# Optimization experiments

Measured on AMD Instinct MI355X. Metric: run time of the kernel, lower is better.

The kernel has to match this reference:

```python
import jax, jax.numpy as jnp
import numpy as np

D_MODEL = 256
D_STATE = 64
MAX_CONCEPTS = 64
CENTROID_LR = 0.1
CREATE_THRESHOLD = 0.75
REFINE_THRESHOLD = 1.0
NEG_INF = -1e9


def _l2norm(v):
    # F.normalize with eps=1e-12
    n = jnp.sqrt(jnp.sum(v * v, axis=-1, keepdims=True))
    return v / jnp.maximum(n, 1e-12)


def setup_inputs() -> dict:
    key = jax.random.key(0)
    ks = jax.random.split(key, 6)
    B, T = 4, 1024
    x = jax.random.normal(ks[0], (B, T, D_MODEL), dtype=jnp.float32)
    s = 1.0 / np.sqrt(D_MODEL)
    Wq = jax.random.normal(ks[1], (D_MODEL, D_STATE), dtype=jnp.float32) * s
    Wk = jax.random.normal(ks[2], (D_MODEL, D_STATE), dtype=jnp.float32) * s
    Wv = jax.random.normal(ks[3], (D_MODEL, D_MODEL), dtype=jnp.float32) * s
    Wo = jax.random.normal(ks[4], (D_MODEL, D_MODEL), dtype=jnp.float32) * s
    return {
        "x": x,
        "Wq": Wq, "bq": jnp.zeros((D_STATE,), jnp.float32),
        "Wk": Wk, "bk": jnp.zeros((D_STATE,), jnp.float32),
        "Wv": Wv, "bv": jnp.zeros((D_MODEL,), jnp.float32),
        "Wo": Wo, "bo": jnp.zeros((D_MODEL,), jnp.float32),
        "logit_scale": jnp.float32(np.log(1.0 / np.sqrt(D_STATE))),
    }


def _forward(x, Wq, bq, Wk, bk, Wv, bv, Wo, bo, logit_scale):
    M = MAX_CONCEPTS
    # q is only ever used .detach()ed in the original; k is detached too.
    q_all = jax.lax.stop_gradient(_l2norm((x @ Wq + bq).astype(jnp.float32)))
    k_all = jax.lax.stop_gradient(_l2norm((x @ Wk + bk).astype(jnp.float32)))
    v_all = x @ Wv + bv
    scale = jnp.minimum(jnp.exp(logit_scale), 100.0)
    slot_ids = jnp.arange(M)

    def step(carry, inp):
        centroids, values, counts, n = carry  # [M,ds],[M,dm],[M], int32
        q_t, k_t, v_t = inp
        valid = slot_ids < n
        sims = centroids @ q_t                      # [M]
        scores = jnp.where(valid, sims, NEG_INF)
        weights = jax.nn.softmax(scores * scale)    # [M]
        has = n > 0
        z = jnp.where(has, weights @ values, jnp.zeros_like(v_t))
        sel = jnp.argmax(weights)
        sel_sim = sims[sel]
        v_sel = values[sel]
        residual = jnp.sqrt(jnp.mean(
            (jax.lax.stop_gradient(v_sel) - jax.lax.stop_gradient(v_t)) ** 2))
        refine = has & (n < M) & ((sel_sim < CREATE_THRESHOLD) | (residual > REFINE_THRESHOLD))
        do_add = ((~has) | refine) & (n < M)
        do_update = has & (~refine)
        # running-mean update of value memory; EMA + renormalize of centroid
        upd_c = jax.lax.stop_gradient(
            _l2norm((1.0 - CENTROID_LR) * centroids[sel] + CENTROID_LR * k_t))
        new_v = (v_sel * counts[sel] + v_t) / (counts[sel] + 1.0)
        centroids = centroids.at[sel].set(jnp.where(do_update, upd_c, centroids[sel]))
        values = values.at[sel].set(jnp.where(do_update, new_v, v_sel))
        counts = counts.at[sel].set(counts[sel] + do_update.astype(counts.dtype))
        # concept creation in slot n (sel < n always, so no collision)
        slot = jnp.minimum(n, M - 1)
        centroids = centroids.at[slot].set(jnp.where(do_add, k_t, centroids[slot]))
        values = values.at[slot].set(jnp.where(do_add, v_t, values[slot]))
        counts = counts.at[slot].set(jnp.where(do_add, 1.0, counts[slot]))
        n = n + do_add.astype(n.dtype)
        return (centroids, values, counts, n), z

    def run_seq(q, k, v):
        ds, dm = q.shape[-1], v.shape[-1]
        init = (jnp.zeros((M, ds), jnp.float32),
                jnp.zeros((M, dm), jnp.float32),
                jnp.zeros((M,), jnp.float32),
                jnp.int32(0))
        _, zs = jax.lax.scan(step, init, (q, k, v))
        return zs  # [T, dm]

    y = jax.vmap(run_seq)(q_all, k_all, v_all).astype(x.dtype)
    return y @ Wo + bo  # dropout p=0 -> identity


def reference(x, Wq, bq, Wk, bk, Wv, bv, Wo, bo, logit_scale):
    return _forward(x, Wq, bq, Wk, bk, Wv, bv, Wo, bo, logit_scale)
```

## Files before the change

kernel.cpp:

```cpp
#include <hip/hip_runtime.h>
#include <hip/hip_bf16.h>

#define D_MODEL 256
#define D_STATE 64
#define MCON    64
#define TLEN    1024
#define BATCH   4
#define NEG_INF -1e9f
#define PT      16
#define ZT      8

#define BAR() asm volatile("s_waitcnt lgkmcnt(0)\n\ts_barrier" ::: "memory")

template <int CTRL, int RM>
__device__ __forceinline__ float dpp_f(float x) {
    int xi = __float_as_int(x);
    int r  = __builtin_amdgcn_update_dpp(xi, xi, CTRL, RM, 0xf, false);
    return __int_as_float(r);
}
__device__ __forceinline__ float bcast_lane(float x, int lane) {
    return __int_as_float(__builtin_amdgcn_readlane(__float_as_int(x), lane));
}
__device__ __forceinline__ float wave_sum(float x) {
    x += dpp_f<0x111, 0xf>(x);
    x += dpp_f<0x112, 0xf>(x);
    x += dpp_f<0x114, 0xf>(x);
    x += dpp_f<0x118, 0xf>(x);
    x += dpp_f<0x142, 0xa>(x);
    x += dpp_f<0x143, 0xc>(x);
    return bcast_lane(x, 63);
}
__device__ __forceinline__ float wave_max(float x) {
    x = fmaxf(x, dpp_f<0x111, 0xf>(x));
    x = fmaxf(x, dpp_f<0x112, 0xf>(x));
    x = fmaxf(x, dpp_f<0x114, 0xf>(x));
    x = fmaxf(x, dpp_f<0x118, 0xf>(x));
    x = fmaxf(x, dpp_f<0x142, 0xa>(x));
    x = fmaxf(x, dpp_f<0x143, 0xc>(x));
    return bcast_lane(x, 63);
}
__device__ __forceinline__ int wave_argmax_fast(float lg, float mx) {
    const unsigned long long m = __ballot(lg == mx);
    return (int)(__ffsll((long long)m) - 1);
}
__device__ __forceinline__ float dpp_swap1(float x) {
    int xi = __float_as_int(x);
    return __int_as_float(__builtin_amdgcn_update_dpp(xi, xi, 0xB1, 0xf, 0xf, false));
}

__global__ __launch_bounds__(256) void proj_kernel(
    const float* __restrict__ x,
    const float* __restrict__ Wq, const float* __restrict__ bq,
    const float* __restrict__ Wk, const float* __restrict__ bk,
    const float* __restrict__ Wv, const float* __restrict__ bv,
    float* __restrict__ q_ws, float* __restrict__ k_ws, float* __restrict__ v_ws)
{
    const int tok0 = blockIdx.x * PT;
    const int tid  = threadIdx.x;
    __shared__ float sx[PT][D_MODEL];

    #pragma unroll
    for (int tt = 0; tt < PT; ++tt)
        sx[tt][tid] = x[(size_t)(tok0 + tt) * D_MODEL + tid];
    __syncthreads();

    {
        float acc[PT];
        #pragma unroll
        for (int tt = 0; tt < PT; ++tt) acc[tt] = 0.f;
        for (int i = 0; i < D_MODEL; ++i) {
            const float w = Wv[i * D_MODEL + tid];
            #pragma unroll
            for (int tt = 0; tt < PT; ++tt) acc[tt] += sx[tt][i] * w;
        }
        const float bvi = bv[tid];
        #pragma unroll
        for (int tt = 0; tt < PT; ++tt)
            v_ws[(size_t)(tok0 + tt) * D_MODEL + tid] = acc[tt] + bvi;
    }

    if (tid < 128) {
        const int j = tid & 63;
        const float* W  = (tid < 64) ? Wq : Wk;
        const float* bb = (tid < 64) ? bq : bk;
        float a[PT];
        #pragma unroll
        for (int tt = 0; tt < PT; ++tt) a[tt] = 0.f;
        for (int i = 0; i < D_MODEL; ++i) {
            const float w = W[i * D_STATE + j];
            #pragma unroll
            for (int tt = 0; tt < PT; ++tt) a[tt] += sx[tt][i] * w;
        }
        const float bbj = bb[j];
        #pragma unroll
        for (int tt = 0; tt < PT; ++tt) {
            const float av = a[tt] + bbj;
            float s2 = av * av;
            #pragma unroll
            for (int off = 1; off < 64; off <<= 1) s2 += __shfl_xor(s2, off, 64);
            const float nrm = fmaxf(sqrtf(s2), 1e-12f);
            const float o = av / nrm;
            if (tid < 64) q_ws[(size_t)(tok0 + tt) * D_STATE + j] = o;
            else          k_ws[(size_t)(tok0 + tt) * D_STATE + j] = o;
        }
    }
}

__global__ __launch_bounds__(256) void scan_kernel(
    const float* __restrict__ q_ws, const float* __restrict__ k_ws,
    const float* __restrict__ v_ws,
    float* __restrict__ sims_ws, int* __restrict__ n_ws,
    int* __restrict__ ver_ws, float* __restrict__ vlog_ws,
    const float* __restrict__ ls_p)
{
    const int b   = blockIdx.x;
    const int tid = threadIdx.x;
    const int l   = tid & 63;
    const int wv  = tid >> 6;
    const float scale = fminf(expf(ls_p[0]), 100.f);

    __shared__ __align__(16) float sV[MCON * D_MODEL];
    __shared__ __align__(16) float sQ[2][D_STATE];
    __shared__ __align__(16) float sK[2][D_STATE];
    __shared__ __align__(16) float sBuf[2][MCON];
    __shared__ __align__(16) float sS2[2][MCON];
    __shared__ float sFA[2];
    __shared__ int   sFlagChg[2];
    __shared__ int   sFlagUpd[2];

    const float4 zero4 = make_float4(0.f, 0.f, 0.f, 0.f);
    #pragma unroll
    for (int i = 0; i < 16; ++i) ((float4*)sV)[i * 256 + tid] = zero4;
    if (tid < MCON) { sBuf[0][tid] = 0.f; sS2[0][tid] = 0.f; }
    if (tid == 0) { sFA[0] = 0.f; sFlagChg[0] = -1; sFlagUpd[0] = 0; }

    const float* qg = q_ws + b * TLEN * D_STATE;
    const float* kg = k_ws + b * TLEN * D_STATE;
    const float* vg = v_ws + b * TLEN * D_MODEL;
    float* vlog_b   = vlog_ws + (size_t)b * (TLEN + 1) * D_MODEL;

    if (tid < 64) {
        *(float4*)&vlog_b[4 * l] = zero4;
        sQ[1][l] = qg[D_STATE + l];
        sK[0][l] = kg[l];
    }

    float qcur = 0.f, kcur = 0.f, qnx2 = 0.f, knx = 0.f;
    float fa_prev = 0.f;
    int   n0 = 0, ver0 = 0;
    if (wv == 0) {
        kcur = kg[l];
        qcur = qg[D_STATE + l];
        knx  = kg[D_STATE + l];
        qnx2 = qg[2 * D_STATE + l];
    }
    float  cnt_l = 0.f;
    int    n = 0, chg_prev = -1, upd_prev = 0;
    float4 vvt = zero4;
    if (wv == 1) vvt = *(const float4*)&vg[4 * l];
    const int brow = ((wv - 2) << 5) + (l >> 1);
    const int bh   = l & 1;
    float4 Creg[8];
    float4 tprev[8], kprev[8];
    float  s2prev = 0.f;
    #pragma unroll
    for (int c = 0; c < 8; ++c) { Creg[c] = zero4; tprev[c] = zero4; kprev[c] = zero4; }

    __syncthreads();

    for (int t = 0; t < TLEN; ++t) {
        const int token = b * TLEN + t;
        const int pc = t & 1, pn = 1 - pc;

        if (wv >= 2) {
            const int  chg  = sFlagChg[pc];
            const bool updf = sFlagUpd[pc] != 0;
            if (chg == brow) {
                const float rn = 1.f / fmaxf(sqrtf(s2prev), 1e-12f);
                #pragma unroll
                for (int c = 0; c < 8; ++c) {
                    Creg[c].x = updf ? tprev[c].x * rn : kprev[c].x;
                    Creg[c].y = updf ? tprev[c].y * rn : kprev[c].y;
                    Creg[c].z = updf ? tprev[c].z * rn : kprev[c].z;
                    Creg[c].w = updf ? tprev[c].w * rn : kprev[c].w;
                }
            }
            const float* qrow = &sQ[pn][32 * bh];
            const float* krow = &sK[pc][32 * bh];
            float pa = 0.f, pb = 0.f, sa = 0.f, sb = 0.f;
            #pragma unroll
            for (int c = 0; c < 8; ++c) {
                const float4 c4 = Creg[c];
                const float4 q4 = *(const float4*)(qrow + 4 * c);
                const float4 k4 = *(const float4*)(krow + 4 * c);
                float4 t4;
                t4.x = 0.9f * c4.x + 0.1f * k4.x;
                t4.y = 0.9f * c4.y + 0.1f * k4.y;
                t4.z = 0.9f * c4.z + 0.1f * k4.z;
                t4.w = 0.9f * c4.w + 0.1f * k4.w;
                if (c < 4) {
                    pa += c4.x * q4.x; pa += c4.y * q4.y;
                    pa += c4.z * q4.z; pa += c4.w * q4.w;
                    sa += t4.x * t4.x; sa += t4.y * t4.y;
                    sa += t4.z * t4.z; sa += t4.w * t4.w;
                } else {
                    pb += c4.x * q4.x; pb += c4.y * q4.y;
                    pb += c4.z * q4.z; pb += c4.w * q4.w;
                    sb += t4.x * t4.x; sb += t4.y * t4.y;
                    sb += t4.z * t4.z; sb += t4.w * t4.w;
                }
                tprev[c] = t4; kprev[c] = k4;
            }
            const float sd  = pa + pb;
            const float dot = sd + dpp_swap1(sd);
            const float ss  = sa + sb;
            const float s2  = ss + dpp_swap1(ss);
            s2prev = s2;
            if (bh == 0) { sBuf[pn][brow] = dot; sS2[pn][brow] = s2; }
        }

        if (wv == 0) {
            const int chg0 = sFlagChg[pc];
            const int upd0 = sFlagUpd[pc];
            n0  += (chg0 >= 0 && upd0 == 0) ? 1 : 0;
            if (l == chg0) ver0 = t;
            const float bufv0 = sBuf[pc][l];
            const int   ip0   = (chg0 < 0) ? 0 : chg0;
            const float s2v0  = sS2[pc][ip0];
            const float bdc0  = bcast_lane(bufv0, ip0);
            const float fupd0 = (0.9f * bdc0 + 0.1f * fa_prev)
                                / fmaxf(sqrtf(s2v0), 1e-12f);
            const float fsim0 = upd0 ? fupd0 : fa_prev;
            const float simv0 = (l == chg0) ? fsim0 : bufv0;
            sims_ws[(size_t)token * MCON + l] = simv0;
            ver_ws[(size_t)token * MCON + l]  = ver0;
            if (l == 0) n_ws[token] = n0;

            sQ[pc][l] = qnx2;
            sK[pn][l] = knx;
            const float fa = wave_sum(kcur * qcur);
            if (l == 0) sFA[pn] = fa;
            fa_prev = fa;
            kcur = knx; qcur = qnx2;
            const int tk2 = (t + 2 < TLEN) ? t + 2 : TLEN - 1;
            const int tq3 = (t + 3 < TLEN) ? t + 3 : TLEN - 1;
            knx  = kg[tk2 * D_STATE + l];
            qnx2 = qg[tq3 * D_STATE + l];
        }

        if (wv == 1) {
            const float4 vt = vvt;
            const int tk = (t + 1 < TLEN) ? t + 1 : t;
            vvt = *(const float4*)&vg[tk * D_MODEL + 4 * l];

            const int   ip   = (chg_prev < 0) ? 0 : chg_prev;
            const float bufv = sBuf[pc][l];
            const float s2v  = sS2[pc][ip];
            const float fa   = sFA[pc];
            const float bdc  = bcast_lane(bufv, ip);
            const float fupd = (0.9f * bdc + 0.1f * fa)
                               / fmaxf(sqrtf(s2v), 1e-12f);
            const float fsim = upd_prev ? fupd : fa;
            const float simv = (l == chg_prev) ? fsim : bufv;

            const float lg = ((l < n) ? simv : NEG_INF) * scale;
            const float mx = wave_max(lg);
            const int   sel    = wave_argmax_fast(lg, mx);
            const float selSim = bcast_lane(simv,  sel);
            const float cnt    = bcast_lane(cnt_l, sel);

            const float4 vs = *(const float4*)&sV[sel * D_MODEL + 4 * l];
            float r = (vs.x - vt.x) * (vs.x - vt.x)
                    + (vs.y - vt.y) * (vs.y - vt.y)
                    + (vs.z - vt.z) * (vs.z - vt.z)
                    + (vs.w - vt.w) * (vs.w - vt.w);
            const float residual = sqrtf(wave_sum(r) * (1.f / 256.f));

            const bool has = n > 0;
            const bool refine = has && (n < MCON) &&
                                (selSim < 0.75f || residual > 1.0f);
            const bool do_add    = ((!has) || refine) && (n < MCON);
            const bool do_update = has && !refine;
            const int  chg = do_update ? sel : n;

            float4 nv;
            nv.x = (vs.x * cnt + vt.x) / (cnt + 1.f);
            nv.y = (vs.y * cnt + vt.y) / (cnt + 1.f);
            nv.z = (vs.z * cnt + vt.z) / (cnt + 1.f);
            nv.w = (vs.w * cnt + vt.w) / (cnt + 1.f);
            float4 valV;
            valV.x = do_update ? nv.x : vt.x;
            valV.y = do_update ? nv.y : vt.y;
            valV.z = do_update ? nv.z : vt.z;
            valV.w = do_update ? nv.w : vt.w;
            *(float4*)&sV[chg * D_MODEL + 4 * l] = valV;
            *(float4*)&vlog_b[(size_t)(t + 1) * D_MODEL + 4 * l] = valV;

            if (l == 0) { sFlagChg[pn] = chg; sFlagUpd[pn] = do_update ? 1 : 0; }

            if (l == sel && do_update) cnt_l = cnt + 1.f;
            if (l == n   && do_add)    cnt_l = 1.f;
            n += do_add ? 1 : 0;
            chg_prev = chg; upd_prev = do_update ? 1 : 0;
        }

        BAR();
    }
}

__global__ __launch_bounds__(256) void zout_kernel(
    const float* __restrict__ sims_ws, const int* __restrict__ n_ws,
    const int* __restrict__ ver_ws, const float* __restrict__ vlog_ws,
    const float* __restrict__ Wo, const float* __restrict__ bo,
    float* __restrict__ out, const float* __restrict__ ls_p)
{
    const int tok0 = blockIdx.x * ZT;
    const int b    = tok0 >> 10;
    const int tid  = threadIdx.x;
    const int l    = tid & 63;
    const int wv   = tid >> 6;
    const float scale = fminf(expf(ls_p[0]), 100.f);

    __shared__ float sWt[ZT][MCON];
    __shared__ int   sVer[ZT][MCON];
    __shared__ int   sN[ZT];
    __shared__ float sy[ZT][D_MODEL];

    for (int tt = wv; tt < ZT; tt += 4) {
        const int token = tok0 + tt;
        const int nt = n_ws[token];
        if (l == 0) sN[tt] = nt;
        sVer[tt][l] = ver_ws[(size_t)token * MCON + l];
        const float simv = sims_ws[(size_t)token * MCON + l];
        const float lg = ((l < nt) ? simv : NEG_INF) * scale;
        const float mx = wave_max(lg);
        const float e  = expf(lg - mx);
        const float sm = wave_sum(e);
        sWt[tt][l] = e / sm;
    }
    __syncthreads();

    const float* base = vlog_ws + (size_t)b * (TLEN + 1) * D_MODEL;
    #pragma unroll
    for (int tt = 0; tt < ZT; ++tt) {
        float z = 0.f;
        const int ntc = sN[tt];
        if (ntc > 0) {
            #pragma unroll 8
            for (int m = 0; m < ntc; ++m) {
                const float wm = sWt[tt][m];
                z += wm * base[(size_t)sVer[tt][m] * D_MODEL + tid];
            }
        }
        sy[tt][tid] = z;
    }
    __syncthreads();

    float acc[ZT];
    #pragma unroll
    for (int tt = 0; tt < ZT; ++tt) acc[tt] = 0.f;
    for (int i = 0; i < D_MODEL; ++i) {
        const float wo = Wo[i * D_MODEL + tid];
        #pragma unroll
        for (int tt = 0; tt < ZT; ++tt) acc[tt] += sy[tt][i] * wo;
    }
    const float boi = bo[tid];
    #pragma unroll
    for (int tt = 0; tt < ZT; ++tt)
        out[(size_t)(tok0 + tt) * D_MODEL + tid] = acc[tt] + boi;
}

extern "C" void kernel_launch(void* const* d_in, const int* in_sizes, int n_in,
                              void* d_out, int out_size, void* d_ws, size_t ws_size,
                              hipStream_t stream)
{
    const float* x  = (const float*)d_in[0];
    const float* Wq = (const float*)d_in[1];
    const float* bq = (const float*)d_in[2];
    const float* Wk = (const float*)d_in[3];
    const float* bk = (const float*)d_in[4];
    const float* Wv = (const float*)d_in[5];
    const float* bv = (const float*)d_in[6];
    const float* Wo = (const float*)d_in[7];
    const float* bo = (const float*)d_in[8];
    const float* ls = (const float*)d_in[9];
    float* out = (float*)d_out;

    const int NTOK = BATCH * TLEN;
    char* ws = (char*)d_ws;
    size_t off = 0;
    float* q_ws    = (float*)(ws + off); off += (size_t)NTOK * D_STATE * 4;
    float* k_ws    = (float*)(ws + off); off += (size_t)NTOK * D_STATE * 4;
    float* v_ws    = (float*)(ws + off); off += (size_t)NTOK * D_MODEL * 4;
    float* sims_ws = (float*)(ws + off); off += (size_t)NTOK * MCON * 4;
    int*   ver_ws  = (int*)  (ws + off); off += (size_t)NTOK * MCON * 4;
    int*   n_ws    = (int*)  (ws + off); off += (size_t)NTOK * 4;
    float* vlog_ws = (float*)(ws + off);

    proj_kernel<<<NTOK / PT, 256, 0, stream>>>(x, Wq, bq, Wk, bk, Wv, bv,
                                               q_ws, k_ws, v_ws);
    scan_kernel<<<BATCH, 256, 0, stream>>>(q_ws, k_ws, v_ws,
                                           sims_ws, n_ws, ver_ws, vlog_ws, ls);
    zout_kernel<<<NTOK / ZT, 256, 0, stream>>>(sims_ws, n_ws, ver_ws, vlog_ws,
                                               Wo, bo, out, ls);
}
```

Baseline: 846.1 us.

## Fuse scan and output kernels with flag-based overlap of zout chunks

Merges the sequential scan kernel and the output projection kernel into one persistent launch. The first blocks run the per-batch scan and post release flags every 64 tokens, while the remaining blocks spin on those flags and compute softmax-weighted outputs and the Wo projection for finished chunks. The aim is to hide the output stage behind the long serial scan. This relies on all blocks being co-resident and adds spin-wait and fence overhead, with a fallback to separate launches when the workspace is too small.

After: 869.8 us. +2.8%, slower.

```diff
diff --git a/kernel.cpp b/kernel.cpp
--- a/kernel.cpp
+++ b/kernel.cpp
@@ -9,6 +9,9 @@
 #define NEG_INF -1e9f
 #define PT      16
 #define ZT      8
+#define ZUNITS  512
+#define NZB     508
+#define SMEM_BYTES 67616
 
 #define BAR() asm volatile("s_waitcnt lgkmcnt(0)\n\ts_barrier" ::: "memory")
 
@@ -46,6 +49,10 @@
 __device__ __forceinline__ float dpp_swap1(float x) {
     int xi = __float_as_int(x);
     return __int_as_float(__builtin_amdgcn_update_dpp(xi, xi, 0xB1, 0xf, 0xf, false));
+}
+
+__device__ __forceinline__ void post_flag(int* f) {
+    __hip_atomic_store(f, 1, __ATOMIC_RELEASE, __HIP_MEMORY_SCOPE_AGENT);
 }
 
 __global__ __launch_bounds__(256) void proj_kernel(
@@ -106,32 +113,33 @@
     }
 }
 
-__global__ __launch_bounds__(256) void scan_kernel(
+template <bool SYNC>
+__device__ __forceinline__ void scan_role(
+    int b, char* smem,
     const float* __restrict__ q_ws, const float* __restrict__ k_ws,
     const float* __restrict__ v_ws,
     float* __restrict__ sims_ws, int* __restrict__ n_ws,
     int* __restrict__ ver_ws, float* __restrict__ vlog_ws,
-    const float* __restrict__ ls_p)
-{
-    const int b   = blockIdx.x;
+    const float* __restrict__ ls_p, int* sflag)
+{
     const int tid = threadIdx.x;
     const int l   = tid & 63;
     const int wv  = tid >> 6;
     const float scale = fminf(expf(ls_p[0]), 100.f);
 
-    __shared__ __align__(16) float sV[MCON * D_MODEL];
-    __shared__ __align__(16) float sQ[2][D_STATE];
-    __shared__ __align__(16) float sK[2][D_STATE];
-    __shared__ __align__(16) float sBuf[2][MCON];
-    __shared__ __align__(16) float sS2[2][MCON];
-    __shared__ float sFA[2];
-    __shared__ int   sFlagChg[2];
-    __shared__ int   sFlagUpd[2];
+    float* sV       = (float*)smem;
+    float* sQ       = (float*)(smem + 65536);
+    float* sK       = (float*)(smem + 66048);
+    float* sBuf     = (float*)(smem + 66560);
+    float* sS2      = (float*)(smem + 67072);
+    float* sFA      = (float*)(smem + 67584);
+    int*   sFlagChg = (int*)  (smem + 67592);
+    int*   sFlagUpd = (int*)  (smem + 67600);
 
     const float4 zero4 = make_float4(0.f, 0.f, 0.f, 0.f);
     #pragma unroll
     for (int i = 0; i < 16; ++i) ((float4*)sV)[i * 256 + tid] = zero4;
-    if (tid < MCON) { sBuf[0][tid] = 0.f; sS2[0][tid] = 0.f; }
+    if (tid < MCON) { sBuf[tid] = 0.f; sS2[tid] = 0.f; }
     if (tid == 0) { sFA[0] = 0.f; sFlagChg[0] = -1; sFlagUpd[0] = 0; }
 
     const float* qg = q_ws + b * TLEN * D_STATE;
@@ -141,8 +149,8 @@
 
     if (tid < 64) {
         *(float4*)&vlog_b[4 * l] = zero4;
-        sQ[1][l] = qg[D_STATE + l];
-        sK[0][l] = kg[l];
+        sQ[64 + l] = qg[D_STATE + l];
+        sK[l]      = kg[l];
     }
 
     float qcur = 0.f, kcur = 0.f, qnx2 = 0.f, knx = 0.f;
@@ -185,8 +193,8 @@
                     Creg[c].w = updf ? tprev[c].w * rn : kprev[c].w;
                 }
             }
-            const float* qrow = &sQ[pn][32 * bh];
-            const float* krow = &sK[pc][32 * bh];
+            const float* qrow = sQ + pn * 64 + 32 * bh;
+            const float* krow = sK + pc * 64 + 32 * bh;
             float pa = 0.f, pb = 0.f, sa = 0.f, sb = 0.f;
             #pragma unroll
             for (int c = 0; c < 8; ++c) {
@@ -216,17 +224,23 @@
             const float ss  = sa + sb;
             const float s2  = ss + dpp_swap1(ss);
             s2prev = s2;
-            if (bh == 0) { sBuf[pn][brow] = dot; sS2[pn][brow] = s2; }
+            if (bh == 0) { sBuf[pn * 64 + brow] = dot; sS2[pn * 64 + brow] = s2; }
         }
 
         if (wv == 0) {
+            if constexpr (SYNC) {
+                if ((t & 63) == 0 && t != 0) {
+                    __threadfence();
+                    if (l == 0) post_flag(&sflag[b * 16 + (t >> 6) - 1]);
+                }
+            }
             const int chg0 = sFlagChg[pc];
             const int upd0 = sFlagUpd[pc];
             n0  += (chg0 >= 0 && upd0 == 0) ? 1 : 0;
             if (l == chg0) ver0 = t;
-            const float bufv0 = sBuf[pc][l];
+            const float bufv0 = sBuf[pc * 64 + l];
             const int   ip0   = (chg0 < 0) ? 0 : chg0;
-            const float s2v0  = sS2[pc][ip0];
+            const float s2v0  = sS2[pc * 64 + ip0];
             const float bdc0  = bcast_lane(bufv0, ip0);
             const float fupd0 = (0.9f * bdc0 + 0.1f * fa_prev)
                                 / fmaxf(sqrtf(s2v0), 1e-12f);
@@ -236,8 +250,8 @@
             ver_ws[(size_t)token * MCON + l]  = ver0;
             if (l == 0) n_ws[token] = n0;
 
-            sQ[pc][l] = qnx2;
-            sK[pn][l] = knx;
+            sQ[pc * 64 + l] = qnx2;
+            sK[pn * 64 + l] = knx;
             const float fa = wave_sum(kcur * qcur);
             if (l == 0) sFA[pn] = fa;
             fa_prev = fa;
@@ -252,10 +266,14 @@
             const float4 vt = vvt;
             const int tk = (t + 1 < TLEN) ? t + 1 : t;
             vvt = *(const float4*)&vg[tk * D_MODEL + 4 * l];
+            if constexpr (SYNC) {
+                if ((t & 63) == 63)
+                    asm volatile("s_waitcnt vmcnt(1)" ::: "memory");
+            }
 
             const int   ip   = (chg_prev < 0) ? 0 : chg_prev;
-            const float bufv = sBuf[pc][l];
-            const float s2v  = sS2[pc][ip];
+            const float bufv = sBuf[pc * 64 + l];
+            const float s2v  = sS2[pc * 64 + ip];
             const float fa   = sFA[pc];
             const float bdc  = bcast_lane(bufv, ip);
             const float fupd = (0.9f * bdc + 0.1f * fa)
@@ -306,25 +324,45 @@
 
         BAR();
     }
-}
-
-__global__ __launch_bounds__(256) void zout_kernel(
+
+    if constexpr (SYNC) {
+        if (wv == 0) {
+            __threadfence();
+            if (l == 0) post_flag(&sflag[b * 16 + 15]);
+        }
+    }
+}
+
+template <bool WAIT>
+__device__ __forceinline__ void zout_unit(
+    int u, char* smem,
     const float* __restrict__ sims_ws, const int* __restrict__ n_ws,
     const int* __restrict__ ver_ws, const float* __restrict__ vlog_ws,
     const float* __restrict__ Wo, const float* __restrict__ bo,
-    float* __restrict__ out, const float* __restrict__ ls_p)
-{
-    const int tok0 = blockIdx.x * ZT;
+    float* __restrict__ out, float scale, const int* sflag)
+{
+    const int tok0 = u * ZT;
     const int b    = tok0 >> 10;
     const int tid  = threadIdx.x;
     const int l    = tid & 63;
     const int wv   = tid >> 6;
-    const float scale = fminf(expf(ls_p[0]), 100.f);
-
-    __shared__ float sWt[ZT][MCON];
-    __shared__ int   sVer[ZT][MCON];
-    __shared__ int   sN[ZT];
-    __shared__ float sy[ZT][D_MODEL];
+
+    if constexpr (WAIT) {
+        const int* f = &sflag[b * 16 + ((tok0 & 1023) >> 6)];
+        if (tid == 0) {
+            while (__hip_atomic_load(f, __ATOMIC_RELAXED,
+                                     __HIP_MEMORY_SCOPE_AGENT) == 0)
+                __builtin_amdgcn_s_sleep(32);
+            (void)__hip_atomic_load(f, __ATOMIC_ACQUIRE,
+                                    __HIP_MEMORY_SCOPE_AGENT);
+        }
+        __syncthreads();
+    }
+
+    float (*sWt)[MCON]   = (float(*)[MCON])smem;
+    int   (*sVer)[MCON]  = (int(*)[MCON])(smem + 2048);
+    int*    sN           = (int*)(smem + 4096);
+    float (*sy)[D_MODEL] = (float(*)[D_MODEL])(smem + 4160);
 
     for (int tt = wv; tt < ZT; tt += 4) {
         const int token = tok0 + tt;
@@ -368,6 +406,52 @@
     #pragma unroll
     for (int tt = 0; tt < ZT; ++tt)
         out[(size_t)(tok0 + tt) * D_MODEL + tid] = acc[tt] + boi;
+    __syncthreads();
+}
+
+__global__ __launch_bounds__(256, 2) void scan_zout_kernel(
+    const float* __restrict__ q_ws, const float* __restrict__ k_ws,
+    const float* __restrict__ v_ws,
+    float* __restrict__ sims_ws, int* __restrict__ n_ws,
+    int* __restrict__ ver_ws, float* __restrict__ vlog_ws,
+    const float* __restrict__ Wo, const float* __restrict__ bo,
+    float* __restrict__ out, const float* __restrict__ ls_p,
+    int* sflag)
+{
+    __shared__ __align__(16) char smem[SMEM_BYTES];
+    const int bid = blockIdx.x;
+    if (bid < BATCH) {
+        scan_role<true>(bid, smem, q_ws, k_ws, v_ws,
+                        sims_ws, n_ws, ver_ws, vlog_ws, ls_p, sflag);
+    } else {
+        const float scale = fminf(expf(ls_p[0]), 100.f);
+        const int zb = bid - BATCH;
+        zout_unit<true>(zb, smem, sims_ws, n_ws, ver_ws, vlog_ws,
+                        Wo, bo, out, scale, sflag);
+        if (zb < ZUNITS - NZB) {
+            zout_unit<true>(NZB + zb, smem, sims_ws, n_ws, ver_ws, vlog_ws,
+                            Wo, bo, out, scale, sflag);
+        }
+    }
+}
+
+__global__ __launch_bounds__(256) void scan_fb(
+    const float* q_ws, const float* k_ws, const float* v_ws,
+    float* sims_ws, int* n_ws, int* ver_ws, float* vlog_ws, const float* ls)
+{
+    __shared__ __align__(16) char smem[SMEM_BYTES];
+    scan_role<false>(blockIdx.x, smem, q_ws, k_ws, v_ws,
+                     sims_ws, n_ws, ver_ws, vlog_ws, ls, nullptr);
+}
+__global__ __launch_bounds__(256) void zout_fb(
+    const float* sims_ws, const int* n_ws, const int* ver_ws,
+    const float* vlog_ws, const float* Wo, const float* bo,
+    float* out, const float* ls)
+{
+    __shared__ __align__(16) char smem[12352];
+    const float scale = fminf(expf(ls[0]), 100.f);
+    zout_unit<false>(blockIdx.x, smem, sims_ws, n_ws, ver_ws, vlog_ws,
+                     Wo, bo, out, scale, nullptr);
 }
 
 extern "C" void kernel_launch(void* const* d_in, const int* in_sizes, int n_in,
@@ -396,11 +480,20 @@
     int*   ver_ws  = (int*)  (ws + off); off += (size_t)NTOK * MCON * 4;
     int*   n_ws    = (int*)  (ws + off); off += (size_t)NTOK * 4;
     float* vlog_ws = (float*)(ws + off);
+    off += (size_t)BATCH * (TLEN + 1) * D_MODEL * 4;
+    int*   sflag   = (int*)(ws + off); off += BATCH * 16 * 4;
 
     proj_kernel<<<NTOK / PT, 256, 0, stream>>>(x, Wq, bq, Wk, bk, Wv, bv,
                                                q_ws, k_ws, v_ws);
-    scan_kernel<<<BATCH, 256, 0, stream>>>(q_ws, k_ws, v_ws,
+    if (ws_size >= off) {
+        hipMemsetAsync(sflag, 0, BATCH * 16 * 4, stream);
+        scan_zout_kernel<<<BATCH + NZB, 256, 0, stream>>>(
+            q_ws, k_ws, v_ws, sims_ws, n_ws, ver_ws, vlog_ws,
+            Wo, bo, out, ls, sflag);
+    } else {
+        scan_fb<<<BATCH, 256, 0, stream>>>(q_ws, k_ws, v_ws,
                                            sims_ws, n_ws, ver_ws, vlog_ws, ls);
-    zout_kernel<<<NTOK / ZT, 256, 0, stream>>>(sims_ws, n_ws, ver_ws, vlog_ws,
-                                               Wo, bo, out, ls);
-}
+        zout_fb<<<ZUNITS, 256, 0, stream>>>(sims_ws, n_ws, ver_ws, vlog_ws,
+                                            Wo, bo, out, ls);
+    }
+}
```
